# Kernel tuning notes

Measured on AMD Instinct MI355X. Metric: run time of the kernel, lower is better.

## Reference

```python
import jax, jax.numpy as jnp
import numpy as np
import math

B, T, C = 16, 1029, 1024
H, D = 16, 64  # n_heads, head_dim
NPH = NPW = 32  # 32x32 patch grid -> 1024 patch tokens
ROPE_BASE = 100.0


def _rope_cos_sin():
    # DINOv3 patch-center coordinates in [-1, 1]
    ch = (np.arange(0.5, NPH, dtype=np.float32) / NPH)
    cw = (np.arange(0.5, NPW, dtype=np.float32) / NPW)
    coords = np.stack(np.meshgrid(ch, cw, indexing='ij'), axis=-1).reshape(-1, 2)  # [N,2]
    coords = 2.0 * coords - 1.0
    inv_freq = 1.0 / ROPE_BASE ** np.arange(0, 1, 4.0 / D, dtype=np.float32)  # [D/4]
    angles = 2.0 * math.pi * coords[:, :, None] * inv_freq[None, None, :]  # [N,2,D/4]
    angles = angles.reshape(-1, D // 2)  # [N, D/2]
    angles = np.tile(angles, (1, 2))  # [N, D]
    return jnp.asarray(np.cos(angles)), jnp.asarray(np.sin(angles))


def setup_inputs() -> dict:
    key = jax.random.key(0)
    ks = jax.random.split(key, 6)
    s = 1.0 / math.sqrt(C)
    cos, sin = _rope_cos_sin()
    return {
        'x': jax.random.normal(ks[0], (B, T, C), jnp.float32),
        'Wqkv': jax.random.normal(ks[1], (C, 3 * C), jnp.float32) * s,
        'bqkv': jax.random.normal(ks[2], (3 * C,), jnp.float32) * 0.02,
        'Wout': jax.random.normal(ks[3], (C, C), jnp.float32) * s,
        'bout': jax.random.normal(ks[4], (C,), jnp.float32) * 0.02,
        'cos': cos,
        'sin': sin,
        'num_prefix': 5,  # 1 CLS + 4 registers
    }


def _rotate_half(t):
    t1, t2 = jnp.split(t, 2, axis=-1)
    return jnp.concatenate((-t2, t1), axis=-1)


def reference(x, Wqkv, bqkv, Wout, bout, cos, sin, num_prefix):
    Bx, Tx, Cx = x.shape
    qkv = x @ Wqkv + bqkv  # [B,T,3C]
    q, k, v = jnp.split(qkv, 3, axis=-1)
    to_heads = lambda t: t.reshape(Bx, Tx, H, D).transpose(0, 2, 1, 3)  # [B,H,T,D]
    q, k, v = to_heads(q), to_heads(k), to_heads(v)

    # RoPE on patch tokens only (skip CLS/register prefix)
    qp = q[:, :, num_prefix:] * cos + _rotate_half(q[:, :, num_prefix:]) * sin
    kp = k[:, :, num_prefix:] * cos + _rotate_half(k[:, :, num_prefix:]) * sin
    q = jnp.concatenate((q[:, :, :num_prefix], qp), axis=2)
    k = jnp.concatenate((k[:, :, :num_prefix], kp), axis=2)

    scale = 1.0 / math.sqrt(D)
    attn = jax.nn.softmax(jnp.einsum('bhqd,bhkd->bhqk', q, k) * scale, axis=-1)
    y = jnp.einsum('bhqk,bhkd->bhqd', attn, v)  # [B,H,T,D]
    y = y.transpose(0, 2, 1, 3).reshape(Bx, Tx, Cx)
    return y @ Wout + bout
```

## Files before the change

### kernel.cpp

```cpp
#include <hip/hip_runtime.h>
#include <hip/hip_bf16.h>
#include <stdint.h>

typedef __bf16 bf16;
typedef bf16 bf16x8 __attribute__((ext_vector_type(8)));
typedef bf16 bf16x4 __attribute__((ext_vector_type(4)));
typedef float f32x4 __attribute__((ext_vector_type(4)));

#define DEV static __device__ __forceinline__

constexpr int Bc = 16, Tc = 1029, Cc = 1024, Hc = 16, Dc = 64;
constexpr int KPAD = 1088;
constexpr int QPAD = 1152;
constexpr int MPAD = 16640;
constexpr int NKT  = KPAD / 64;
constexpr int NVT  = KPAD / 32;

DEV void gload16(void* lds_dst, const void* gsrc) {
  __builtin_amdgcn_global_load_lds(
      (const __attribute__((address_space(1))) void*)gsrc,
      (__attribute__((address_space(3))) void*)lds_dst, 16, 0, 0);
}

__global__ __launch_bounds__(256) void cast_x(const float* __restrict__ x,
                                              bf16* __restrict__ xb) {
  const size_t i = ((size_t)blockIdx.x * 256 + threadIdx.x) * 8;
  const int row = (int)(i >> 10);
  bf16x8 o = {};
  if (row < Bc * Tc) {
    const float4* p = (const float4*)(x + i);
    float4 a = p[0], b = p[1];
    o[0] = (bf16)a.x; o[1] = (bf16)a.y; o[2] = (bf16)a.z; o[3] = (bf16)a.w;
    o[4] = (bf16)b.x; o[5] = (bf16)b.y; o[6] = (bf16)b.z; o[7] = (bf16)b.w;
  }
  *(bf16x8*)(xb + i) = o;
}

__global__ __launch_bounds__(256) void transpose_cast(const float* __restrict__ W,
                                                      bf16* __restrict__ Wt,
                                                      int rows, int cols) {
  __shared__ float tile[32][33];
  const int c0 = blockIdx.x * 32;
  const int r0 = blockIdx.y * 32;
  const int tr = threadIdx.x >> 5;
  const int tc = threadIdx.x & 31;
#pragma unroll
  for (int j = 0; j < 4; ++j)
    tile[tr + j * 8][tc] = W[(size_t)(r0 + tr + j * 8) * cols + c0 + tc];
  __syncthreads();
#pragma unroll
  for (int j = 0; j < 4; ++j)
    Wt[(size_t)(c0 + tr + j * 8) * rows + r0 + tc] = (bf16)tile[tc][tr + j * 8];
}

template <bool OUT_BF16>
__global__ __launch_bounds__(512, 2) void gemm256(const bf16* __restrict__ A,
                                                  const bf16* __restrict__ Bt,
                                                  const float* __restrict__ bias,
                                                  void* __restrict__ Cout,
                                                  int N, int K, int Mlim,
                                                  int nblk_n) {
  __shared__ bf16 As[2][256 * 64];
  __shared__ bf16 Bs[2][256 * 64];
  const int tid = threadIdx.x;
  const int lane = tid & 63;
  const int w = tid >> 6;
  const int wm = w >> 2;
  const int wn = w & 3;
  const int g = lane >> 4, c = lane & 15;

  const int nwg = gridDim.x;
  const int orig = blockIdx.x;
  const int q = nwg >> 3, r = nwg & 7;
  const int xcd = orig & 7;
  const int idx = (xcd < r ? xcd * (q + 1) : r * (q + 1) + (xcd - r) * q) + (orig >> 3);
  const int m0 = (idx / nblk_n) * 256;
  const int n0 = (idx % nblk_n) * 256;

  auto stage = [&](int buf, int k0) {
#pragma unroll
    for (int j = 0; j < 4; ++j) {
      const int id2 = j * 512 + tid;
      const int row = id2 >> 3, ch = id2 & 7;
      const int sc = (ch ^ (row & 7)) << 4;
      gload16((char*)&As[buf][0] + id2 * 16,
              (const char*)(A + (size_t)(m0 + row) * K + k0) + sc);
    }
#pragma unroll
    for (int j = 0; j < 4; ++j) {
      const int id2 = j * 512 + tid;
      const int row = id2 >> 3, ch = id2 & 7;
      const int sc = (ch ^ (row & 7)) << 4;
      gload16((char*)&Bs[buf][0] + id2 * 16,
              (const char*)(Bt + (size_t)(n0 + row) * K + k0) + sc);
    }
  };

  f32x4 acc[8][4] = {};

  stage(0, 0);
  stage(1, 64);
  asm volatile("s_waitcnt vmcnt(8)" ::: "memory");
  __builtin_amdgcn_s_barrier();

  const int nk = K / 64;
  for (int kt = 0; kt < nk; ++kt) {
    const int buf = kt & 1;

    bf16x8 af[8][2], bq[4][2];
#pragma unroll
    for (int mi = 0; mi < 8; ++mi) {
      const int row = wm * 128 + mi * 16 + c;
#pragma unroll
      for (int kc = 0; kc < 2; ++kc) {
        const int chn = (kc * 4 + g) ^ (row & 7);
        af[mi][kc] = *(const bf16x8*)((const char*)&As[buf][0] + row * 128 + chn * 16);
      }
    }
#pragma unroll
    for (int nj = 0; nj < 4; ++nj) {
      const int row = wn * 64 + nj * 16 + c;
#pragma unroll
      for (int kc = 0; kc < 2; ++kc) {
        const int chn = (kc * 4 + g) ^ (row & 7);
        bq[nj][kc] = *(const bf16x8*)((const char*)&Bs[buf][0] + row * 128 + chn * 16);
      }
    }

    asm volatile("s_waitcnt lgkmcnt(0)" ::: "memory");
    __builtin_amdgcn_sched_barrier(0);
    __builtin_amdgcn_s_barrier();
    __builtin_amdgcn_sched_barrier(0);

    if (kt + 2 < nk) stage(buf, (kt + 2) * 64);
    __builtin_amdgcn_sched_barrier(0);

    __builtin_amdgcn_s_setprio(1);
#pragma unroll
    for (int kc = 0; kc < 2; ++kc)
#pragma unroll
      for (int mi = 0; mi < 8; ++mi)
#pragma unroll
        for (int nj = 0; nj < 4; ++nj)
          acc[mi][nj] = __builtin_amdgcn_mfma_f32_16x16x32_bf16(
              af[mi][kc], bq[nj][kc], acc[mi][nj], 0, 0, 0);
    __builtin_amdgcn_s_setprio(0);

    if (kt + 2 < nk)
      asm volatile("s_waitcnt vmcnt(8)" ::: "memory");
    else
      asm volatile("s_waitcnt vmcnt(0)" ::: "memory");
    __builtin_amdgcn_sched_barrier(0);
    __builtin_amdgcn_s_barrier();
  }

#pragma unroll
  for (int mi = 0; mi < 8; ++mi) {
    const int mb = m0 + wm * 128 + mi * 16 + g * 4;
#pragma unroll
    for (int nj = 0; nj < 4; ++nj) {
      const int n = n0 + wn * 64 + nj * 16 + c;
      const float bv = bias[n];
#pragma unroll
      for (int r2 = 0; r2 < 4; ++r2) {
        const int m = mb + r2;
        if (m < Mlim) {
          const float v = acc[mi][nj][r2] + bv;
          if constexpr (OUT_BF16)
            ((bf16*)Cout)[(size_t)m * N + n] = (bf16)v;
          else
            ((float*)Cout)[(size_t)m * N + n] = v;
        }
      }
    }
  }
}

template <bool OUT_BF16>
__global__ __launch_bounds__(256) void gemm_bt(const bf16* __restrict__ A,
                                               const bf16* __restrict__ Bt,
                                               const float* __restrict__ bias,
                                               void* __restrict__ Cout,
                                               int N, int K, int Mlim) {
  constexpr int BM = 128, BN = 128, BK = 32;
  __shared__ bf16 As[2][BM * BK];
  __shared__ bf16 Bs[2][BN * BK];
  const int tid  = threadIdx.x;
  const int lane = tid & 63;
  const int wave = tid >> 6;
  const int g = lane >> 4;
  const int c = lane & 15;
  const int m0 = blockIdx.y * BM;
  const int n0 = blockIdx.x * BN;
  const int wm = (wave >> 1) * 64;
  const int wn = (wave & 1) * 64;

  auto stage = [&](int buf, int k0) {
#pragma unroll
    for (int j = 0; j < 2; ++j) {
      int idx = j * 256 + tid;
      int row = idx >> 2, ch = idx & 3;
      int sc = ((ch ^ ((row >> 1) & 3)) << 4);
      gload16((char*)&As[buf][0] + idx * 16,
              (const char*)(A + (size_t)(m0 + row) * K + k0) + sc);
    }
#pragma unroll
    for (int j = 0; j < 2; ++j) {
      int idx = j * 256 + tid;
      int row = idx >> 2, ch = idx & 3;
      int sc = ((ch ^ ((row >> 1) & 3)) << 4);
      gload16((char*)&Bs[buf][0] + idx * 16,
              (const char*)(Bt + (size_t)(n0 + row) * K + k0) + sc);
    }
  };

  f32x4 acc[4][4] = {};
  stage(0, 0);
  __syncthreads();
  const int nk = K / BK;
  for (int kt = 0; kt < nk; ++kt) {
    const int buf = kt & 1;
    if (kt + 1 < nk) stage(buf ^ 1, (kt + 1) * BK);
    bf16x8 af[4], bfr[4];
#pragma unroll
    for (int i = 0; i < 4; ++i) {
      const int ra = wm + i * 16 + c;
      const int rb = wn + i * 16 + c;
      af[i]  = *(const bf16x8*)((const char*)&As[buf][0] + ra * 64 +
                                (((g ^ ((ra >> 1) & 3)) << 4)));
      bfr[i] = *(const bf16x8*)((const char*)&Bs[buf][0] + rb * 64 +
                                (((g ^ ((rb >> 1) & 3)) << 4)));
    }
#pragma unroll
    for (int i = 0; i < 4; ++i)
#pragma unroll
      for (int j = 0; j < 4; ++j)
        acc[i][j] = __builtin_amdgcn_mfma_f32_16x16x32_bf16(af[i], bfr[j], acc[i][j], 0, 0, 0);
    __syncthreads();
  }

#pragma unroll
  for (int i = 0; i < 4; ++i) {
    const int mb = m0 + wm + i * 16 + g * 4;
#pragma unroll
    for (int j = 0; j < 4; ++j) {
      const int n = n0 + wn + j * 16 + c;
      const float bv = bias[n];
#pragma unroll
      for (int r = 0; r < 4; ++r) {
        const int m = mb + r;
        if (m < Mlim) {
          float v = acc[i][j][r] + bv;
          if constexpr (OUT_BF16)
            ((bf16*)Cout)[(size_t)m * N + n] = (bf16)v;
          else
            ((float*)Cout)[(size_t)m * N + n] = v;
        }
      }
    }
  }
}

__global__ __launch_bounds__(256) void rope_qk(const bf16* __restrict__ qkv,
                                               const float* __restrict__ cosT,
                                               const float* __restrict__ sinT,
                                               const int* __restrict__ npfx_p,
                                               bf16* __restrict__ Qh,
                                               bf16* __restrict__ Kh) {
  const int bt = blockIdx.x;
  const int b = bt / QPAD, t = bt % QPAD;
  const int h  = threadIdx.x >> 4;
  const int d0 = (threadIdx.x & 15) * 4;
  const size_t qoff = (((size_t)(b * Hc + h)) * QPAD + t) * Dc + d0;
  const size_t koff = (((size_t)(b * Hc + h)) * KPAD + t) * Dc + d0;
  if (t >= Tc) {
    bf16x4 z = {};
    *(bf16x4*)(Qh + qoff) = z;
    if (t < KPAD) *(bf16x4*)(Kh + koff) = z;
    return;
  }
  const int npfx = *npfx_p;
  const size_t inb = ((size_t)b * Tc + t) * 3072 + h * Dc;
  bf16x4 qv = *(const bf16x4*)(qkv + inb + d0);
  bf16x4 kv = *(const bf16x4*)(qkv + inb + 1024 + d0);
  float q[4], k[4];
#pragma unroll
  for (int u = 0; u < 4; ++u) { q[u] = (float)qv[u]; k[u] = (float)kv[u]; }
  if (t >= npfx) {
    const int p  = t - npfx;
    const int dp = (d0 < 32) ? d0 + 32 : d0 - 32;
    const float sgn = (d0 < 32) ? -1.f : 1.f;
    bf16x4 qp = *(const bf16x4*)(qkv + inb + dp);
    bf16x4 kp = *(const bf16x4*)(qkv + inb + 1024 + dp);
    float4 csv = *(const float4*)(cosT + (size_t)p * Dc + d0);
    float4 snv = *(const float4*)(sinT + (size_t)p * Dc + d0);
    float cs[4] = {csv.x, csv.y, csv.z, csv.w};
    float sn[4] = {snv.x, snv.y, snv.z, snv.w};
#pragma unroll
    for (int u = 0; u < 4; ++u) {
      q[u] = q[u] * cs[u] + sgn * (float)qp[u] * sn[u];
      k[u] = k[u] * cs[u] + sgn * (float)kp[u] * sn[u];
    }
  }
  bf16x4 qo, ko;
#pragma unroll
  for (int u = 0; u < 4; ++u) {
    qo[u] = (bf16)(q[u] * 0.18033688f);
    ko[u] = (bf16)k[u];
  }
  *(bf16x4*)(Qh + qoff) = qo;
  *(bf16x4*)(Kh + koff) = ko;
}

__global__ __launch_bounds__(256) void vtrans(const bf16* __restrict__ qkv,
                                              bf16* __restrict__ Vt) {
  __shared__ bf16 lds[64][40];
  const int blk = blockIdx.x;
  const int tt = blk % NVT;
  const int bh = blk / NVT;
  const int b = bh >> 4, h = bh & 15;
  const int t0 = tt * 32;
  const int tl = threadIdx.x >> 3;
  const int ch = threadIdx.x & 7;
  bf16x8 v = {};
  const int t = t0 + tl;
  if (t < Tc)
    v = *(const bf16x8*)(qkv + ((size_t)b * Tc + t) * 3072 + 2048 + h * Dc + ch * 8);
#pragma unroll
  for (int u = 0; u < 8; ++u) lds[ch * 8 + u][tl] = v[u];
  __syncthreads();
  const int d  = threadIdx.x >> 2;
  const int tc = threadIdx.x & 3;
  bf16x8 o = *(const bf16x8*)&lds[d][tc * 8];
  *(bf16x8*)(Vt + ((size_t)bh * Dc + d) * KPAD + t0 + tc * 8) = o;
}

__global__ __launch_bounds__(256, 3) void attn4(const bf16* __restrict__ Qh,
                                                const bf16* __restrict__ Kh,
                                                const bf16* __restrict__ Vt,
                                                bf16* __restrict__ y2d) {
  __shared__ bf16 Ks[2][64 * 64];
  __shared__ bf16 Vs[2][64 * 64];
  __shared__ bf16 Ps[4][32 * 64];
  const int bh = blockIdx.y;
  const int b = bh >> 4, h = bh & 15;
  const int tid = threadIdx.x;
  const int w = tid >> 6, lane = tid & 63;
  const int g = lane >> 4, c = lane & 15;
  const int q0 = blockIdx.x * 128 + w * 32;
  const bf16* Qb = Qh + (size_t)bh * QPAD * Dc;
  const bf16* Kb = Kh + (size_t)bh * KPAD * Dc;
  const bf16* Vb = Vt + (size_t)bh * Dc * KPAD;
  char* Pw = (char*)&Ps[w][0];

  auto stage = [&](int buf, int k0) {
#pragma unroll
    for (int j = 0; j < 2; ++j) {
      int idx = j * 256 + tid;
      int row = idx >> 3;
      int scb = ((idx & 7) << 4) ^ ((row & 7) << 4);
      gload16((char*)&Ks[buf][0] + idx * 16,
              (const char*)(Kb + (size_t)(k0 + row) * 64) + scb);
    }
#pragma unroll
    for (int j = 0; j < 2; ++j) {
      int idx = j * 256 + tid;
      int row = idx >> 3;
      int scb = ((idx & 7) << 4) ^ ((row & 7) << 4);
      gload16((char*)&Vs[buf][0] + idx * 16,
              (const char*)(Vb + (size_t)row * KPAD + k0) + scb);
    }
  };

  bf16x8 qf[2][2];
#pragma unroll
  for (int fm = 0; fm < 2; ++fm)
#pragma unroll
    for (int kc = 0; kc < 2; ++kc)
      qf[fm][kc] = *(const bf16x8*)(Qb + (size_t)(q0 + fm * 16 + c) * Dc + kc * 32 + g * 8);

  bf16x8 ones;
#pragma unroll
  for (int u = 0; u < 8; ++u) ones[u] = (bf16)1.0f;

  float mrun[2] = {-1e30f, -1e30f}, lrun[2] = {0.f, 0.f};
  f32x4 oacc[2][4] = {};

  stage(0, 0);
  __syncthreads();

  for (int kt = 0; kt < NKT; ++kt) {
    const int buf = kt & 1;
    const int k0 = kt * 64;
    if (kt + 1 < NKT) stage(buf ^ 1, (kt + 1) * 64);

    f32x4 st[4][2] = {};
    __builtin_amdgcn_s_setprio(1);
#pragma unroll
    for (int fn = 0; fn < 4; ++fn) {
      const int row = fn * 16 + c;
      const int sw = (row & 7) << 4;
#pragma unroll
      for (int kc = 0; kc < 2; ++kc) {
        bf16x8 kf = *(const bf16x8*)((const char*)&Ks[buf][0] + row * 128 +
                                     ((kc * 64 + g * 16) ^ sw));
#pragma unroll
        for (int fm = 0; fm < 2; ++fm)
          st[fn][fm] = __builtin_amdgcn_mfma_f32_16x16x32_bf16(kf, qf[fm][kc], st[fn][fm], 0, 0, 0);
      }
    }
    __builtin_amdgcn_s_setprio(0);

    if (k0 + 64 > Tc) {
#pragma unroll
      for (int fn = 0; fn < 4; ++fn)
#pragma unroll
        for (int r = 0; r < 4; ++r)
          if (k0 + fn * 16 + g * 4 + r >= Tc) {
            st[fn][0][r] = -1e30f;
            st[fn][1][r] = -1e30f;
          }
    }

    float mx[2];
#pragma unroll
    for (int fm = 0; fm < 2; ++fm) {
      float m0 = fmaxf(fmaxf(st[0][fm][0], st[0][fm][1]), fmaxf(st[0][fm][2], st[0][fm][3]));
      float m1 = fmaxf(fmaxf(st[1][fm][0], st[1][fm][1]), fmaxf(st[1][fm][2], st[1][fm][3]));
      float m2 = fmaxf(fmaxf(st[2][fm][0], st[2][fm][1]), fmaxf(st[2][fm][2], st[2][fm][3]));
      float m3 = fmaxf(fmaxf(st[3][fm][0], st[3][fm][1]), fmaxf(st[3][fm][2], st[3][fm][3]));
      float m = fmaxf(fmaxf(m0, m1), fmaxf(m2, m3));
      m = fmaxf(m, __shfl_xor(m, 16));
      m = fmaxf(m, __shfl_xor(m, 32));
      mx[fm] = m;
    }
    const bool ok = (mx[0] - mrun[0] <= 11.f) && (mx[1] - mrun[1] <= 11.f);
    if (!__all(ok)) {
#pragma unroll
      for (int fm = 0; fm < 2; ++fm) {
        const float mnew = fmaxf(mrun[fm], mx[fm]);
        const float al = __builtin_amdgcn_exp2f(mrun[fm] - mnew);
        mrun[fm] = mnew;
        lrun[fm] *= al;
#pragma unroll
        for (int fd = 0; fd < 4; ++fd) oacc[fm][fd] *= al;
      }
    }
#pragma unroll
    for (int fm = 0; fm < 2; ++fm) {
      const int row = fm * 16 + c;
      const int sw = (row & 7) << 4;
#pragma unroll
      for (int fn = 0; fn < 4; ++fn) {
        bf16x4 pv;
#pragma unroll
        for (int r = 0; r < 4; ++r)
          pv[r] = (bf16)__builtin_amdgcn_exp2f(st[fn][fm][r] - mrun[fm]);
        *(bf16x4*)(Pw + row * 128 + ((fn * 32 + g * 8) ^ sw)) = pv;
      }
    }

    bf16x8 pf[2][2];
    f32x4 ps2[2] = {};
#pragma unroll
    for (int fm = 0; fm < 2; ++fm) {
      const int row = fm * 16 + c;
      const int sw = (row & 7) << 4;
#pragma unroll
      for (int kc = 0; kc < 2; ++kc) {
        pf[fm][kc] = *(const bf16x8*)(Pw + row * 128 + ((kc * 64 + g * 16) ^ sw));
        ps2[fm] = __builtin_amdgcn_mfma_f32_16x16x32_bf16(ones, pf[fm][kc], ps2[fm], 0, 0, 0);
      }
    }
    __builtin_amdgcn_s_setprio(1);
#pragma unroll
    for (int fd = 0; fd < 4; ++fd) {
      const int row = fd * 16 + c;
      const int sw = (row & 7) << 4;
#pragma unroll
      for (int kc = 0; kc < 2; ++kc) {
        bf16x8 vf = *(const bf16x8*)((const char*)&Vs[buf][0] + row * 128 +
                                     ((kc * 64 + g * 16) ^ sw));
#pragma unroll
        for (int fm = 0; fm < 2; ++fm)
          oacc[fm][fd] = __builtin_amdgcn_mfma_f32_16x16x32_bf16(vf, pf[fm][kc], oacc[fm][fd], 0, 0, 0);
      }
    }
    __builtin_amdgcn_s_setprio(0);
#pragma unroll
    for (int fm = 0; fm < 2; ++fm) lrun[fm] += ps2[fm][0];
    __syncthreads();
  }

#pragma unroll
  for (int fm = 0; fm < 2; ++fm) {
    const int trow = q0 + fm * 16 + c;
    if (trow < Tc) {
      const float inv = 1.f / lrun[fm];
#pragma unroll
      for (int fd = 0; fd < 4; ++fd) {
        bf16x4 ov;
#pragma unroll
        for (int r = 0; r < 4; ++r) ov[r] = (bf16)(oacc[fm][fd][r] * inv);
        *(bf16x4*)(y2d + ((size_t)b * Tc + trow) * Cc + h * Dc + fd * 16 + g * 4) = ov;
      }
    }
  }
}

extern "C" void kernel_launch(void* const* d_in, const int* in_sizes, int n_in,
                              void* d_out, int out_size, void* d_ws, size_t ws_size,
                              hipStream_t stream) {
  const float* x    = (const float*)d_in[0];
  const float* Wqkv = (const float*)d_in[1];
  const float* bqkv = (const float*)d_in[2];
  const float* Wout = (const float*)d_in[3];
  const float* bout = (const float*)d_in[4];
  const float* cosT = (const float*)d_in[5];
  const float* sinT = (const float*)d_in[6];
  const int*   npfx = (const int*)d_in[7];

  char* ws = (char*)d_ws;
  size_t off = 0;
  auto alloc = [&](size_t bytes) {
    char* p = ws + off;
    off = (off + bytes + 255) & ~(size_t)255;
    return p;
  };
  bf16* xb  = (bf16*)alloc((size_t)MPAD * 1024 * 2);
  bf16* Wt1 = (bf16*)alloc((size_t)3072 * 1024 * 2);
  bf16* Wt2 = (bf16*)alloc((size_t)1024 * 1024 * 2);
  bf16* qkv = (bf16*)alloc((size_t)MPAD * 3072 * 2);
  bf16* Qh  = (bf16*)alloc((size_t)256 * QPAD * 64 * 2);
  bf16* Kh  = (bf16*)alloc((size_t)256 * KPAD * 64 * 2);
  bf16* Vt  = (bf16*)alloc((size_t)256 * KPAD * 64 * 2);
  bf16* y2d = xb;
  if (off > ws_size) return;

  cast_x<<<dim3(MPAD * 1024 / 2048), dim3(256), 0, stream>>>(x, xb);
  transpose_cast<<<dim3(3072 / 32, 1024 / 32), dim3(256), 0, stream>>>(Wqkv, Wt1, 1024, 3072);
  transpose_cast<<<dim3(1024 / 32, 1024 / 32), dim3(256), 0, stream>>>(Wout, Wt2, 1024, 1024);
  gemm256<true><<<dim3((MPAD / 256) * (3072 / 256)), dim3(512), 0, stream>>>(
      xb, Wt1, bqkv, (void*)qkv, 3072, 1024, MPAD, 3072 / 256);
  rope_qk<<<dim3(Bc * QPAD), dim3(256), 0, stream>>>(qkv, cosT, sinT, npfx, Qh, Kh);
  vtrans<<<dim3(256 * NVT), dim3(256), 0, stream>>>(qkv, Vt);
  attn4<<<dim3(QPAD / 128, 256), dim3(256), 0, stream>>>(Qh, Kh, Vt, y2d);
  gemm_bt<false><<<dim3(1024 / 128, MPAD / 128), dim3(256), 0, stream>>>(
      y2d, Wt2, bout, d_out, 1024, 1024, Bc * Tc);
}
```

Baseline: 429.1 us.

## Split GEMM LDS fragment loads into quarters to cut register pressure

The GEMM inner loop now reads its LDS fragments in four smaller groups (4 A and 4 B fragments at a time) and runs the MFMAs for each group, where before it held all 8x2 A and 4x2 B fragments in registers at once. This lowers VGPR use and could allow better occupancy or fewer spills. The prefetch of tile kt+2 is also moved to after all MFMAs and a barrier, which removes its overlap with compute. The extra lgkmcnt(0) waits serialize LDS reads against the MFMAs.

After: 426.0 us. About the same (-0.7%).

```diff
diff --git a/kernel.cpp b/kernel.cpp
--- a/kernel.cpp
+++ b/kernel.cpp
@@ -96,6 +96,17 @@
     }
   };
 
+  auto ldA = [&](int buf, int mi, int kc) -> bf16x8 {
+    const int row = wm * 128 + mi * 16 + c;
+    const int chn = (kc * 4 + g) ^ (row & 7);
+    return *(const bf16x8*)((const char*)&As[buf][0] + row * 128 + chn * 16);
+  };
+  auto ldB = [&](int buf, int nj, int kc) -> bf16x8 {
+    const int row = wn * 64 + nj * 16 + c;
+    const int chn = (kc * 4 + g) ^ (row & 7);
+    return *(const bf16x8*)((const char*)&Bs[buf][0] + row * 128 + chn * 16);
+  };
+
   f32x4 acc[8][4] = {};
 
   stage(0, 0);
@@ -106,50 +117,70 @@
   const int nk = K / 64;
   for (int kt = 0; kt < nk; ++kt) {
     const int buf = kt & 1;
-
-    bf16x8 af[8][2], bq[4][2];
-#pragma unroll
-    for (int mi = 0; mi < 8; ++mi) {
-      const int row = wm * 128 + mi * 16 + c;
-#pragma unroll
-      for (int kc = 0; kc < 2; ++kc) {
-        const int chn = (kc * 4 + g) ^ (row & 7);
-        af[mi][kc] = *(const bf16x8*)((const char*)&As[buf][0] + row * 128 + chn * 16);
-      }
-    }
-#pragma unroll
-    for (int nj = 0; nj < 4; ++nj) {
-      const int row = wn * 64 + nj * 16 + c;
-#pragma unroll
-      for (int kc = 0; kc < 2; ++kc) {
-        const int chn = (kc * 4 + g) ^ (row & 7);
-        bq[nj][kc] = *(const bf16x8*)((const char*)&Bs[buf][0] + row * 128 + chn * 16);
-      }
-    }
-
+    bf16x8 a[4], bq[4];
+
+#pragma unroll
+    for (int mi = 0; mi < 4; ++mi) a[mi] = ldA(buf, mi, 0);
+#pragma unroll
+    for (int nj = 0; nj < 4; ++nj) bq[nj] = ldB(buf, nj, 0);
     asm volatile("s_waitcnt lgkmcnt(0)" ::: "memory");
     __builtin_amdgcn_sched_barrier(0);
+    __builtin_amdgcn_s_setprio(1);
+#pragma unroll
+    for (int mi = 0; mi < 4; ++mi)
+#pragma unroll
+      for (int nj = 0; nj < 4; ++nj)
+        acc[mi][nj] = __builtin_amdgcn_mfma_f32_16x16x32_bf16(a[mi], bq[nj], acc[mi][nj], 0, 0, 0);
+    __builtin_amdgcn_s_setprio(0);
+
+#pragma unroll
+    for (int mi = 0; mi < 4; ++mi) a[mi] = ldA(buf, mi + 4, 0);
+    asm volatile("s_waitcnt lgkmcnt(0)" ::: "memory");
+    __builtin_amdgcn_sched_barrier(0);
+    __builtin_amdgcn_s_setprio(1);
+#pragma unroll
+    for (int mi = 0; mi < 4; ++mi)
+#pragma unroll
+      for (int nj = 0; nj < 4; ++nj)
+        acc[mi + 4][nj] = __builtin_amdgcn_mfma_f32_16x16x32_bf16(a[mi], bq[nj], acc[mi + 4][nj], 0, 0, 0);
+    __builtin_amdgcn_s_setprio(0);
+
+#pragma unroll
+    for (int mi = 0; mi < 4; ++mi) a[mi] = ldA(buf, mi, 1);
+#pragma unroll
+    for (int nj = 0; nj < 4; ++nj) bq[nj] = ldB(buf, nj, 1);
+    asm volatile("s_waitcnt lgkmcnt(0)" ::: "memory");
+    __builtin_amdgcn_sched_barrier(0);
+    __builtin_amdgcn_s_setprio(1);
+#pragma unroll
+    for (int mi = 0; mi < 4; ++mi)
+#pragma unroll
+      for (int nj = 0; nj < 4; ++nj)
+        acc[mi][nj] = __builtin_amdgcn_mfma_f32_16x16x32_bf16(a[mi], bq[nj], acc[mi][nj], 0, 0, 0);
+    __builtin_amdgcn_s_setprio(0);
+
+#pragma unroll
+    for (int mi = 0; mi < 4; ++mi) a[mi] = ldA(buf, mi + 4, 1);
+    asm volatile("s_waitcnt lgkmcnt(0)" ::: "memory");
+    __builtin_amdgcn_sched_barrier(0);
+    __builtin_amdgcn_s_setprio(1);
+#pragma unroll
+    for (int mi = 0; mi < 4; ++mi)
+#pragma unroll
+      for (int nj = 0; nj < 4; ++nj)
+        acc[mi + 4][nj] = __builtin_amdgcn_mfma_f32_16x16x32_bf16(a[mi], bq[nj], acc[mi + 4][nj], 0, 0, 0);
+    __builtin_amdgcn_s_setprio(0);
+
+    __builtin_amdgcn_sched_barrier(0);
     __builtin_amdgcn_s_barrier();
     __builtin_amdgcn_sched_barrier(0);
-
-    if (kt + 2 < nk) stage(buf, (kt + 2) * 64);
-    __builtin_amdgcn_sched_barrier(0);
-
-    __builtin_amdgcn_s_setprio(1);
-#pragma unroll
-    for (int kc = 0; kc < 2; ++kc)
-#pragma unroll
-      for (int mi = 0; mi < 8; ++mi)
-#pragma unroll
-        for (int nj = 0; nj < 4; ++nj)
-          acc[mi][nj] = __builtin_amdgcn_mfma_f32_16x16x32_bf16(
-              af[mi][kc], bq[nj][kc], acc[mi][nj], 0, 0, 0);
-    __builtin_amdgcn_s_setprio(0);
-
-    if (kt + 2 < nk)
+    if (kt + 2 < nk) {
+      stage(buf, (kt + 2) * 64);
+      __builtin_amdgcn_sched_barrier(0);
       asm volatile("s_waitcnt vmcnt(8)" ::: "memory");
-    else
+    } else {
       asm volatile("s_waitcnt vmcnt(0)" ::: "memory");
+    }
     __builtin_amdgcn_sched_barrier(0);
     __builtin_amdgcn_s_barrier();
   }
```
